# Performance work log

Hardware: AMD Instinct MI355X
Metric: run time of the kernel (lower is better)

The kernel has to match this reference:

```python
import jax, jax.numpy as jnp
import numpy as np

B, C, H, W = 2, 256, 64, 64
NH = 4          # num_heads -> ch = C // NH = 64
G = 32          # GroupNorm groups (normalization(channels))
EPS = 1e-5


def setup_inputs() -> dict:
    key = jax.random.key(0)
    ks = jax.random.split(key, 7)
    s = 1.0 / np.sqrt(C).astype(np.float32)
    return {
        "x": jax.random.normal(ks[0], (B, C, H, W), jnp.float32),
        "gn_scale": 1.0 + 0.02 * jax.random.normal(ks[1], (C,), jnp.float32),
        "gn_bias": 0.02 * jax.random.normal(ks[2], (C,), jnp.float32),
        "w_qkv": s * jax.random.normal(ks[3], (3 * C, C), jnp.float32),
        "b_qkv": jnp.zeros((3 * C,), jnp.float32),
        # NOTE: original zero-inits proj_out; we use random weights so the
        # attention path contributes to the output (meaningful baseline).
        "w_proj": s * jax.random.normal(ks[4], (C, C), jnp.float32),
        "b_proj": jnp.zeros((C,), jnp.float32),
    }


def reference(x, gn_scale, gn_bias, w_qkv, b_qkv, w_proj, b_proj):
    b, c = x.shape[0], x.shape[1]
    spatial = x.shape[2:]
    t = int(np.prod(spatial))
    xf = x.reshape(b, c, t)                      # [B, C, T]

    # GroupNorm(32) over (channels-in-group, T)
    xg = xf.reshape(b, G, c // G, t)
    mu = xg.mean(axis=(2, 3), keepdims=True)
    var = xg.var(axis=(2, 3), keepdims=True)
    xn = ((xg - mu) * jax.lax.rsqrt(var + EPS)).reshape(b, c, t)
    xn = xn * gn_scale[None, :, None] + gn_bias[None, :, None]

    # 1x1 conv -> qkv: [B, 3C, T]
    qkv = jnp.einsum('oc,bct->bot', w_qkv, xn) + b_qkv[None, :, None]

    # QKVAttentionLegacy: reshape (B*H, 3*ch, T) then split
    ch = c // NH
    qkv_h = qkv.reshape(b * NH, 3 * ch, t)
    q, k, v = jnp.split(qkv_h, 3, axis=1)        # each [B*H, ch, T]
    scale = 1.0 / np.sqrt(np.sqrt(ch)).astype(np.float32)
    w = jnp.einsum('bct,bcs->bts', q * scale, k * scale)   # [B*H, T, T]
    w = jax.nn.softmax(w.astype(jnp.float32), axis=-1).astype(qkv.dtype)
    a = jnp.einsum('bts,bcs->bct', w, v).reshape(b, c, t)  # [B, C, T]

    # proj 1x1 conv + residual
    h = jnp.einsum('oc,bct->bot', w_proj, a) + b_proj[None, :, None]
    return (xf + h).reshape(b, c, *spatial)
```

## Files before the change

### kernel.cpp

```cpp
#include <hip/hip_runtime.h>
#include <math.h>

#define T 4096
#define C 256
#define BATCH 2
#define NH 4
#define G 32
#define CPG 8
#define EPS 1e-5f
#define LOG2E 1.4426950408889634f
#define QSCALE (0.125f * LOG2E)
#define KSPLIT 4
#define KRANGE (T / KSPLIT)
#define BH (BATCH * NH)

typedef __attribute__((ext_vector_type(8))) short bfv8;
typedef __attribute__((ext_vector_type(4))) short bfv4;
typedef __attribute__((ext_vector_type(4))) float f32x4;
typedef __attribute__((ext_vector_type(16))) float f32x16;

static __device__ __forceinline__ short f2bf(float f) {
    union { float f; unsigned u; } v; v.f = f;
    return (short)((v.u + 0x7FFFu + ((v.u >> 16) & 1u)) >> 16);
}
static __device__ __forceinline__ short f2bf_fast(float f) {
    union { float f; unsigned u; } v; v.f = f;
    return (short)((v.u + 0x8000u) >> 16);
}
static __device__ __forceinline__ float bf2f(short s) {
    union { float f; unsigned u; } v; v.u = ((unsigned)(unsigned short)s) << 16;
    return v.f;
}

#if __has_builtin(__builtin_amdgcn_exp2f)
#define EXP2(x) __builtin_amdgcn_exp2f(x)
#else
#define EXP2(x) exp2f(x)
#endif

#define AS1 __attribute__((address_space(1)))
#define AS3 __attribute__((address_space(3)))
static __device__ __forceinline__ void gll16(const void* g, void* l) {
    __builtin_amdgcn_global_load_lds((const AS1 void*)g, (AS3 void*)l, 16, 0, 0);
}

__global__ __launch_bounds__(256) void prep_w(const float* __restrict__ wq,
                                              const float* __restrict__ wp,
                                              short* __restrict__ wqb,
                                              short* __restrict__ wpb) {
    int i = blockIdx.x * 256 + threadIdx.x;
    const int NQ = 768 * 256 / 4;
    float4 v; short* dst;
    if (i < NQ) { v = ((const float4*)wq)[i]; dst = wqb + i * 4; }
    else        { int j = i - NQ; v = ((const float4*)wp)[j]; dst = wpb + j * 4; }
    bfv4 o = { f2bf(v.x), f2bf(v.y), f2bf(v.z), f2bf(v.w) };
    *(bfv4*)dst = o;
}

__global__ __launch_bounds__(256) void gn_stats(const float* __restrict__ x,
                                                float* __restrict__ gnp) {
    const int blk = blockIdx.x;
    const int ts  = blockIdx.y;
    const int b = blk / G, g = blk % G;
    const float* xp = x + ((size_t)b * C + g * CPG) * T + ts * 1024;

    const int tid = threadIdx.x;
    float s = 0.f, ss = 0.f;
    #pragma unroll
    for (int u = 0; u < CPG; u++) {
        float4 v = ((const float4*)(xp + (size_t)u * T))[tid];
        s  += v.x + v.y + v.z + v.w;
        ss += v.x*v.x + v.y*v.y + v.z*v.z + v.w*v.w;
    }
    __shared__ float rs[256], rss[256];
    rs[tid] = s; rss[tid] = ss;
    __syncthreads();
    for (int off = 128; off > 0; off >>= 1) {
        if (tid < off) { rs[tid] += rs[tid+off]; rss[tid] += rss[tid+off]; }
        __syncthreads();
    }
    if (tid == 0) {
        gnp[(blk * 4 + ts) * 2 + 0] = rs[0];
        gnp[(blk * 4 + ts) * 2 + 1] = rss[0];
    }
}

__global__ __launch_bounds__(256) void gn_norm(const float* __restrict__ x,
                                               const float* __restrict__ scale,
                                               const float* __restrict__ bias,
                                               const float* __restrict__ gnp,
                                               short* __restrict__ xnT) {
    const int blk = blockIdx.x;
    const int ts  = blockIdx.y;
    const int b = blk / G, g = blk % G;
    const int c0 = g * CPG;
    const float* xp = x + ((size_t)b * C + c0) * T;

    float s = 0.f, ss = 0.f;
    #pragma unroll
    for (int i = 0; i < 4; i++) {
        s  += gnp[(blk * 4 + i) * 2 + 0];
        ss += gnp[(blk * 4 + i) * 2 + 1];
    }
    const float inv_n = 1.0f / (CPG * T);
    const float mu  = s * inv_n;
    const float var = ss * inv_n - mu * mu;
    const float rstd = rsqrtf(var + EPS);

    float sc[CPG], bi[CPG];
    #pragma unroll
    for (int u = 0; u < CPG; u++) {
        sc[u] = scale[c0+u] * rstd;
        bi[u] = bias[c0+u] - mu * sc[u];
    }

    const int t = ts * 1024 + threadIdx.x * 4;
    float vv[CPG][4];
    #pragma unroll
    for (int u = 0; u < CPG; u++) {
        float4 v = *(const float4*)&xp[(size_t)u * T + t];
        vv[u][0] = v.x * sc[u] + bi[u];
        vv[u][1] = v.y * sc[u] + bi[u];
        vv[u][2] = v.z * sc[u] + bi[u];
        vv[u][3] = v.w * sc[u] + bi[u];
    }
    #pragma unroll
    for (int j = 0; j < 4; j++) {
        bfv8 w = { f2bf(vv[0][j]), f2bf(vv[1][j]), f2bf(vv[2][j]), f2bf(vv[3][j]),
                   f2bf(vv[4][j]), f2bf(vv[5][j]), f2bf(vv[6][j]), f2bf(vv[7][j]) };
        *(bfv8*)&xnT[((size_t)b * T + t + j) * C + c0] = w;
    }
}

__global__ __launch_bounds__(256) void gemm_qkv(
    const short* __restrict__ wq,
    const float* __restrict__ bq,
    const short* __restrict__ xnT,
    short* __restrict__ qb, short* __restrict__ kb, short* __restrict__ vb)
{
    const int b  = blockIdx.z;
    const int t0 = blockIdx.x * 64;
    const int ot = blockIdx.y;
    const int h = ot / 3, part = ot % 3;
    const int o0 = ot * 64;

    __shared__ short sm[8192];
    short* Ab = sm;
    short* Bb = sm + 4096;

    const int tid = threadIdx.x, lane = tid & 63, wave = tid >> 6;
    const int col = lane & 15, quad = lane >> 4;
    const short* xb = xnT + (size_t)b * T * C;

    f32x4 acc[4];
    #pragma unroll
    for (int g = 0; g < 4; g++) { acc[g][0]=0.f; acc[g][1]=0.f; acc[g][2]=0.f; acc[g][3]=0.f; }

    for (int k0 = 0; k0 < C; k0 += 64) {
        __syncthreads();
        #pragma unroll
        for (int hh = 0; hh < 2; hh++) {
            gll16(wq + (size_t)(o0 + 16*wave + col) * C + k0 + hh*32 + quad*8,
                  Ab + (hh*4 + wave) * 512);
            gll16(xb + (size_t)(t0 + 16*wave + col) * C + k0 + hh*32 + quad*8,
                  Bb + (hh*4 + wave) * 512);
        }
        __syncthreads();
        #pragma unroll
        for (int hh = 0; hh < 2; hh++) {
            bfv8 af = *(const bfv8*)(Ab + (hh*4 + wave) * 512 + lane*8);
            #pragma unroll
            for (int g = 0; g < 4; g++) {
                bfv8 bf = *(const bfv8*)(Bb + (hh*4 + g) * 512 + lane*8);
                acc[g] = __builtin_amdgcn_mfma_f32_16x16x32_bf16(af, bf, acc[g], 0, 0, 0);
            }
        }
    }

    const int olocal = 16*wave + quad*4;
    float bias_r[4];
    #pragma unroll
    for (int r = 0; r < 4; r++) bias_r[r] = bq[o0 + olocal + r];
    const size_t hd = (size_t)(b * NH + h);

    if (part < 2) {
        short* dst = (part == 0 ? qb : kb) + hd * T * 64;
        const float sc = (part == 0) ? QSCALE : 1.0f;
        #pragma unroll
        for (int g = 0; g < 4; g++) {
            int t = t0 + 16*g + col;
            bfv4 w = { f2bf((acc[g][0] + bias_r[0]) * sc),
                       f2bf((acc[g][1] + bias_r[1]) * sc),
                       f2bf((acc[g][2] + bias_r[2]) * sc),
                       f2bf((acc[g][3] + bias_r[3]) * sc) };
            *(bfv4*)&dst[(size_t)t * 64 + olocal] = w;
        }
    } else {
        short* dst = vb + hd * 64 * T;
        #pragma unroll
        for (int g = 0; g < 4; g++)
            #pragma unroll
            for (int r = 0; r < 4; r++)
                dst[(size_t)(olocal + r) * T + t0 + 16*g + col] =
                    f2bf(acc[g][r] + bias_r[r]);
    }
}

__global__ __launch_bounds__(512, 4) void attn_kernel(
    const short* __restrict__ qb,
    const short* __restrict__ kb,
    const short* __restrict__ vb,
    short* __restrict__ opart,
    float* __restrict__ lp)
{
    __shared__ short smem[16384];
    const int bh = blockIdx.y;
    const int ks = blockIdx.z;
    const int t0 = blockIdx.x * 256;
    const int k0base = ks * KRANGE;
    const short* kbh = kb + (size_t)bh * T * 64;
    const short* vbh = vb + (size_t)bh * 64 * T;

    const int tid  = threadIdx.x;
    const int lane = tid & 63;
    const int wave = tid >> 6;
    const int klow = lane & 31;
    const int hi   = lane >> 5;
    const int swz  = klow & 7;

    const int q = t0 + wave*32 + klow;
    const short* qrow = qb + (size_t)bh * T * 64 + (size_t)q * 64;
    bfv8 qf[4];
    #pragma unroll
    for (int s = 0; s < 4; s++) qf[s] = *(const bfv8*)(qrow + s*16 + hi*8);

    f32x16 oacc[2];
    #pragma unroll
    for (int c = 0; c < 2; c++)
        #pragma unroll
        for (int r = 0; r < 16; r++) oacc[c][r] = 0.f;
    float lsum = 0.f;

    const int srow = wave*8 + (lane >> 3);
    const int schunk = lane & 7;
    #define STAGE_KV(buf, s0)                                                   \
        {                                                                       \
            short* kB = smem + (buf) * 8192 + wave * 512;                       \
            gll16(kbh + (size_t)((s0) + srow) * 64 + ((schunk ^ (srow&7))<<3),  \
                  kB);                                                          \
            gll16(vbh + (size_t)srow * T + (s0) + ((schunk ^ (srow&7))<<3),     \
                  kB + 4096);                                                   \
        }

    STAGE_KV(0, k0base)

    for (int it = 0; it < KRANGE/64; it++) {
        __syncthreads();
        if (it + 1 < KRANGE/64) STAGE_KV((it+1) & 1, k0base + (it+1)*64)

        const short* kvb = smem + (it & 1) * 8192;
        const short* kl = kvb + klow*64;
        const short* vl = kvb + 4096 + klow*64 + 4*hi;

        bfv8 pf[2][2];
        #pragma unroll
        for (int kt = 0; kt < 2; kt++) {
            f32x16 sacc;
            #pragma unroll
            for (int r = 0; r < 16; r++) sacc[r] = 0.f;
            #pragma unroll
            for (int s = 0; s < 4; s++) {
                bfv8 kf = *(const bfv8*)(kl + kt*2048 + (((2*s+hi) ^ swz) << 3));
                sacc = __builtin_amdgcn_mfma_f32_32x32x16_bf16(kf, qf[s], sacc, 0, 0, 0);
            }
            #pragma unroll
            for (int u = 0; u < 2; u++) {
                bfv8 pk;
                #pragma unroll
                for (int j = 0; j < 8; j++) {
                    float p = EXP2(sacc[u*8 + j]);
                    lsum += p;
                    pk[j] = f2bf_fast(p);
                }
                pf[kt][u] = pk;
            }
        }

        #pragma unroll
        for (int kc = 0; kc < 4; kc++) {
            #pragma unroll
            for (int c = 0; c < 2; c++) {
                bfv4 v0 = *(const bfv4*)(vl + c*2048 + (((2*kc)   ^ swz) << 3));
                bfv4 v1 = *(const bfv4*)(vl + c*2048 + (((2*kc+1) ^ swz) << 3));
                bfv8 vf = { v0[0], v0[1], v0[2], v0[3],
                            v1[0], v1[1], v1[2], v1[3] };
                oacc[c] = __builtin_amdgcn_mfma_f32_32x32x16_bf16(
                              vf, pf[kc>>1][kc&1], oacc[c], 0, 0, 0);
            }
        }
    }

    lsum += __shfl_xor(lsum, 32);

    const size_t rowbase = (size_t)(ks*BH + bh) * T + t0 + wave*32;
    short* opb = opart + (rowbase + klow) * 64;
    #pragma unroll
    for (int c = 0; c < 2; c++)
        #pragma unroll
        for (int u = 0; u < 4; u++) {
            bfv4 w = { f2bf(oacc[c][4*u+0]), f2bf(oacc[c][4*u+1]),
                       f2bf(oacc[c][4*u+2]), f2bf(oacc[c][4*u+3]) };
            *(bfv4*)(opb + c*32 + u*8 + hi*4) = w;
        }
    if (hi == 0) {
        lp[rowbase + klow] = lsum;
    }
}

__global__ __launch_bounds__(256) void gemm_proj(
    const short* __restrict__ wp,
    const float* __restrict__ bp,
    const short* __restrict__ opart,
    const float* __restrict__ lp,
    const float* __restrict__ x,
    float* __restrict__ out)
{
    const int b  = blockIdx.z;
    const int t0 = blockIdx.x * 64;
    const int o0 = blockIdx.y * 64;

    __shared__ short sm[8192];
    short* Ab = sm;
    short* Bb = sm + 4096;

    const int tid = threadIdx.x, lane = tid & 63, wave = tid >> 6;
    const int col = lane & 15, quad = lane >> 4;

    const int trow = t0 + 16*wave + col;
    float rl4[NH];
    #pragma unroll
    for (int hh = 0; hh < NH; hh++) {
        float ls = 0.f;
        #pragma unroll
        for (int ks = 0; ks < KSPLIT; ks++)
            ls += lp[((size_t)(ks*BH) + b*NH + hh) * T + trow];
        rl4[hh] = 1.0f / ls;
    }

    f32x4 acc[4];
    #pragma unroll
    for (int g = 0; g < 4; g++) { acc[g][0]=0.f; acc[g][1]=0.f; acc[g][2]=0.f; acc[g][3]=0.f; }

    for (int k0 = 0; k0 < C; k0 += 64) {
        __syncthreads();
        #pragma unroll
        for (int hh = 0; hh < 2; hh++) {
            gll16(wp + (size_t)(o0 + 16*wave + col) * C + k0 + hh*32 + quad*8,
                  Ab + (hh*4 + wave) * 512);
            const int chg = k0 + hh*32 + quad*8;
            const int hd = chg >> 6, chin = chg & 63;
            const short* ob = opart + (((size_t)(b*NH + hd)) * T + trow) * 64 + chin;
            float a8[8] = {0.f,0.f,0.f,0.f,0.f,0.f,0.f,0.f};
            #pragma unroll
            for (int ks = 0; ks < KSPLIT; ks++) {
                bfv8 v = *(const bfv8*)(ob + (size_t)ks * BH * T * 64);
                #pragma unroll
                for (int u = 0; u < 8; u++) a8[u] += bf2f(v[u]);
            }
            const float rl = rl4[hd];
            bfv8 pk;
            #pragma unroll
            for (int u = 0; u < 8; u++) pk[u] = f2bf(a8[u] * rl);
            *(bfv8*)(Bb + (hh*4 + wave) * 512 + lane*8) = pk;
        }
        __syncthreads();
        #pragma unroll
        for (int hh = 0; hh < 2; hh++) {
            bfv8 af = *(const bfv8*)(Ab + (hh*4 + wave) * 512 + lane*8);
            #pragma unroll
            for (int g = 0; g < 4; g++) {
                bfv8 bf = *(const bfv8*)(Bb + (hh*4 + g) * 512 + lane*8);
                acc[g] = __builtin_amdgcn_mfma_f32_16x16x32_bf16(af, bf, acc[g], 0, 0, 0);
            }
        }
    }

    const int olocal = 16*wave + quad*4;
    #pragma unroll
    for (int r = 0; r < 4; r++) {
        const int o = o0 + olocal + r;
        const float bias = bp[o];
        const size_t rowoff = ((size_t)b * C + o) * T;
        #pragma unroll
        for (int g = 0; g < 4; g++) {
            const size_t idx = rowoff + t0 + 16*g + col;
            out[idx] = acc[g][r] + bias + x[idx];
        }
    }
}

extern "C" void kernel_launch(void* const* d_in, const int* in_sizes, int n_in,
                              void* d_out, int out_size, void* d_ws, size_t ws_size,
                              hipStream_t stream) {
    (void)in_sizes; (void)n_in; (void)out_size; (void)ws_size;
    const float* x        = (const float*)d_in[0];
    const float* gn_scale = (const float*)d_in[1];
    const float* gn_bias  = (const float*)d_in[2];
    const float* w_qkv    = (const float*)d_in[3];
    const float* b_qkv    = (const float*)d_in[4];
    const float* w_proj   = (const float*)d_in[5];
    const float* b_proj   = (const float*)d_in[6];
    float* out = (float*)d_out;

    short* ws    = (short*)d_ws;
    short* qb    = ws;
    short* kb    = qb  + (size_t)BH * T * 64;
    short* vb    = kb  + (size_t)BH * T * 64;
    short* xnT   = vb  + (size_t)BH * T * 64;
    short* wqb   = xnT + (size_t)BATCH * T * C;
    short* wpb   = wqb + 768 * 256;
    short* opart = wpb + 256 * 256;
    float* lp    = (float*)(opart + (size_t)KSPLIT * BH * T * 64);
    float* gnp   = lp + (size_t)KSPLIT * BH * T;

    prep_w<<<dim3(256), 256, 0, stream>>>(w_qkv, w_proj, wqb, wpb);
    gn_stats<<<dim3(BATCH * G, 4), 256, 0, stream>>>(x, gnp);
    gn_norm<<<dim3(BATCH * G, 4), 256, 0, stream>>>(x, gn_scale, gn_bias, gnp, xnT);
    gemm_qkv<<<dim3(T/64, 12, BATCH), 256, 0, stream>>>(wqb, b_qkv, xnT, qb, kb, vb);
    attn_kernel<<<dim3(T/256, BH, KSPLIT), 512, 0, stream>>>(qb, kb, vb, opart, lp);
    gemm_proj<<<dim3(T/64, 4, BATCH), 256, 0, stream>>>(wpb, b_proj, opart, lp, x, out);
}
```

Measured before the change: 152.4 us.

## Double K/V tile to 128, interleave PV MFMAs with softmax, merge prep kernels

The attention kernel now stages 128-key K/V tiles instead of 64, doubling shared memory to 64KB. This halves the number of barrier/stage iterations, and V gets a 16-way swizzle to match the wider rows. The P·V MFMAs are issued right after each softmax sub-block rather than after all scores, and a packed v_cvt_pk_bf16_f32 conversion plus a two-wide sum replace scalar bf16 rounding. Weight conversion and GroupNorm stats are merged into one launch to cut a kernel launch. The larger LDS footprint may reduce occupancy under launch_bounds(512,4).

```diff
diff --git a/kernel.cpp b/kernel.cpp
--- a/kernel.cpp
+++ b/kernel.cpp
@@ -12,20 +12,19 @@
 #define QSCALE (0.125f * LOG2E)
 #define KSPLIT 4
 #define KRANGE (T / KSPLIT)
+#define KTILE 128
+#define NIT (KRANGE / KTILE)
 #define BH (BATCH * NH)
 
 typedef __attribute__((ext_vector_type(8))) short bfv8;
 typedef __attribute__((ext_vector_type(4))) short bfv4;
 typedef __attribute__((ext_vector_type(4))) float f32x4;
+typedef __attribute__((ext_vector_type(2))) float f32x2;
 typedef __attribute__((ext_vector_type(16))) float f32x16;
 
 static __device__ __forceinline__ short f2bf(float f) {
     union { float f; unsigned u; } v; v.f = f;
     return (short)((v.u + 0x7FFFu + ((v.u >> 16) & 1u)) >> 16);
-}
-static __device__ __forceinline__ short f2bf_fast(float f) {
-    union { float f; unsigned u; } v; v.f = f;
-    return (short)((v.u + 0x8000u) >> 16);
 }
 static __device__ __forceinline__ float bf2f(short s) {
     union { float f; unsigned u; } v; v.u = ((unsigned)(unsigned short)s) << 16;
@@ -44,27 +43,29 @@
     __builtin_amdgcn_global_load_lds((const AS1 void*)g, (AS3 void*)l, 16, 0, 0);
 }
 
-__global__ __launch_bounds__(256) void prep_w(const float* __restrict__ wq,
-                                              const float* __restrict__ wp,
-                                              short* __restrict__ wqb,
-                                              short* __restrict__ wpb) {
-    int i = blockIdx.x * 256 + threadIdx.x;
-    const int NQ = 768 * 256 / 4;
-    float4 v; short* dst;
-    if (i < NQ) { v = ((const float4*)wq)[i]; dst = wqb + i * 4; }
-    else        { int j = i - NQ; v = ((const float4*)wp)[j]; dst = wpb + j * 4; }
-    bfv4 o = { f2bf(v.x), f2bf(v.y), f2bf(v.z), f2bf(v.w) };
-    *(bfv4*)dst = o;
-}
-
-__global__ __launch_bounds__(256) void gn_stats(const float* __restrict__ x,
-                                                float* __restrict__ gnp) {
-    const int blk = blockIdx.x;
-    const int ts  = blockIdx.y;
+__global__ __launch_bounds__(256) void prep_stats(
+    const float* __restrict__ wq, const float* __restrict__ wp,
+    short* __restrict__ wqb, short* __restrict__ wpb,
+    const float* __restrict__ x, float* __restrict__ gnp)
+{
+    __shared__ float rs[256], rss[256];
+    const int bid = blockIdx.x;
+    const int tid = threadIdx.x;
+    if (bid < 256) {
+        int i = bid * 256 + tid;
+        const int NQ = 768 * 256 / 4;
+        float4 v; short* dst;
+        if (i < NQ) { v = ((const float4*)wq)[i]; dst = wqb + i * 4; }
+        else        { int j = i - NQ; v = ((const float4*)wp)[j]; dst = wpb + j * 4; }
+        bfv4 o = { f2bf(v.x), f2bf(v.y), f2bf(v.z), f2bf(v.w) };
+        *(bfv4*)dst = o;
+        return;
+    }
+    const int blk = (bid - 256) >> 2;
+    const int ts  = (bid - 256) & 3;
     const int b = blk / G, g = blk % G;
     const float* xp = x + ((size_t)b * C + g * CPG) * T + ts * 1024;
 
-    const int tid = threadIdx.x;
     float s = 0.f, ss = 0.f;
     #pragma unroll
     for (int u = 0; u < CPG; u++) {
@@ -72,7 +73,6 @@
         s  += v.x + v.y + v.z + v.w;
         ss += v.x*v.x + v.y*v.y + v.z*v.z + v.w*v.w;
     }
-    __shared__ float rs[256], rss[256];
     rs[tid] = s; rss[tid] = ss;
     __syncthreads();
     for (int off = 128; off > 0; off >>= 1) {
@@ -213,7 +213,7 @@
     short* __restrict__ opart,
     float* __restrict__ lp)
 {
-    __shared__ short smem[16384];
+    __shared__ short smem[32768];
     const int bh = blockIdx.y;
     const int ks = blockIdx.z;
     const int t0 = blockIdx.x * 256;
@@ -227,6 +227,7 @@
     const int klow = lane & 31;
     const int hi   = lane >> 5;
     const int swz  = klow & 7;
+    const int vswz = klow & 15;
 
     const int q = t0 + wave*32 + klow;
     const short* qrow = qb + (size_t)bh * T * 64 + (size_t)q * 64;
@@ -239,32 +240,39 @@
     for (int c = 0; c < 2; c++)
         #pragma unroll
         for (int r = 0; r < 16; r++) oacc[c][r] = 0.f;
-    float lsum = 0.f;
-
-    const int srow = wave*8 + (lane >> 3);
-    const int schunk = lane & 7;
+    f32x2 l2 = { 0.f, 0.f };
+
+    const int lr8  = lane >> 3, lc8  = lane & 7;
+    const int lr16 = lane >> 4, lc16 = lane & 15;
     #define STAGE_KV(buf, s0)                                                   \
         {                                                                       \
-            short* kB = smem + (buf) * 8192 + wave * 512;                       \
-            gll16(kbh + (size_t)((s0) + srow) * 64 + ((schunk ^ (srow&7))<<3),  \
-                  kB);                                                          \
-            gll16(vbh + (size_t)srow * T + (s0) + ((schunk ^ (srow&7))<<3),     \
-                  kB + 4096);                                                   \
+            short* base = smem + (buf) * 16384;                                 \
+            const int r0 = (wave*2+0)*8 + lr8;                                  \
+            const int r1 = (wave*2+1)*8 + lr8;                                  \
+            gll16(kbh + (size_t)((s0) + r0) * 64 + ((lc8 ^ (r0&7))<<3),         \
+                  base + (wave*2+0)*512);                                       \
+            gll16(kbh + (size_t)((s0) + r1) * 64 + ((lc8 ^ (r1&7))<<3),         \
+                  base + (wave*2+1)*512);                                       \
+            const int v0r = (wave*2+0)*4 + lr16;                                \
+            const int v1r = (wave*2+1)*4 + lr16;                                \
+            gll16(vbh + (size_t)v0r * T + (s0) + ((lc16 ^ (v0r&15))<<3),        \
+                  base + 8192 + (wave*2+0)*512);                                \
+            gll16(vbh + (size_t)v1r * T + (s0) + ((lc16 ^ (v1r&15))<<3),        \
+                  base + 8192 + (wave*2+1)*512);                                \
         }
 
     STAGE_KV(0, k0base)
 
-    for (int it = 0; it < KRANGE/64; it++) {
-        __syncthreads();
-        if (it + 1 < KRANGE/64) STAGE_KV((it+1) & 1, k0base + (it+1)*64)
-
-        const short* kvb = smem + (it & 1) * 8192;
+    for (int it = 0; it < NIT; it++) {
+        __syncthreads();
+        if (it + 1 < NIT) STAGE_KV((it+1) & 1, k0base + (it+1)*KTILE)
+
+        const short* kvb = smem + (it & 1) * 16384;
         const short* kl = kvb + klow*64;
-        const short* vl = kvb + 4096 + klow*64 + 4*hi;
-
-        bfv8 pf[2][2];
-        #pragma unroll
-        for (int kt = 0; kt < 2; kt++) {
+        const short* vl = kvb + 8192 + klow*128 + 4*hi;
+
+        #pragma unroll
+        for (int kt = 0; kt < 4; kt++) {
             f32x16 sacc;
             #pragma unroll
             for (int r = 0; r < 16; r++) sacc[r] = 0.f;
@@ -275,31 +283,32 @@
             }
             #pragma unroll
             for (int u = 0; u < 2; u++) {
-                bfv8 pk;
+                float p[8];
                 #pragma unroll
-                for (int j = 0; j < 8; j++) {
-                    float p = EXP2(sacc[u*8 + j]);
-                    lsum += p;
-                    pk[j] = f2bf_fast(p);
+                for (int j = 0; j < 8; j++) p[j] = EXP2(sacc[8*u + j]);
+                f32x2 pa = { p[0], p[1] }, pb = { p[2], p[3] };
+                f32x2 pc = { p[4], p[5] }, pd = { p[6], p[7] };
+                l2 += (pa + pb) + (pc + pd);
+                union { unsigned w[4]; bfv8 v; } pk_;
+                #pragma unroll
+                for (int w = 0; w < 4; w++)
+                    asm("v_cvt_pk_bf16_f32 %0, %1, %2"
+                        : "=v"(pk_.w[w]) : "v"(p[2*w]), "v"(p[2*w+1]));
+                const int kc = 2*kt + u;
+                #pragma unroll
+                for (int c = 0; c < 2; c++) {
+                    bfv4 v0 = *(const bfv4*)(vl + c*4096 + (((2*kc)   ^ vswz) << 3));
+                    bfv4 v1 = *(const bfv4*)(vl + c*4096 + (((2*kc+1) ^ vswz) << 3));
+                    bfv8 vf = { v0[0], v0[1], v0[2], v0[3],
+                                v1[0], v1[1], v1[2], v1[3] };
+                    oacc[c] = __builtin_amdgcn_mfma_f32_32x32x16_bf16(
+                                  vf, pk_.v, oacc[c], 0, 0, 0);
                 }
-                pf[kt][u] = pk;
             }
         }
-
-        #pragma unroll
-        for (int kc = 0; kc < 4; kc++) {
-            #pragma unroll
-            for (int c = 0; c < 2; c++) {
-                bfv4 v0 = *(const bfv4*)(vl + c*2048 + (((2*kc)   ^ swz) << 3));
-                bfv4 v1 = *(const bfv4*)(vl + c*2048 + (((2*kc+1) ^ swz) << 3));
-                bfv8 vf = { v0[0], v0[1], v0[2], v0[3],
-                            v1[0], v1[1], v1[2], v1[3] };
-                oacc[c] = __builtin_amdgcn_mfma_f32_32x32x16_bf16(
-                              vf, pf[kc>>1][kc&1], oacc[c], 0, 0, 0);
-            }
-        }
-    }
-
+    }
+
+    float lsum = l2[0] + l2[1];
     lsum += __shfl_xor(lsum, 32);
 
     const size_t rowbase = (size_t)(ks*BH + bh) * T + t0 + wave*32;
@@ -423,8 +432,7 @@
     float* lp    = (float*)(opart + (size_t)KSPLIT * BH * T * 64);
     float* gnp   = lp + (size_t)KSPLIT * BH * T;
 
-    prep_w<<<dim3(256), 256, 0, stream>>>(w_qkv, w_proj, wqb, wpb);
-    gn_stats<<<dim3(BATCH * G, 4), 256, 0, stream>>>(x, gnp);
+    prep_stats<<<dim3(512), 256, 0, stream>>>(w_qkv, w_proj, wqb, wpb, x, gnp);
     gn_norm<<<dim3(BATCH * G, 4), 256, 0, stream>>>(x, gn_scale, gn_bias, gnp, xnT);
     gemm_qkv<<<dim3(T/64, 12, BATCH), 256, 0, stream>>>(wqb, b_qkv, xnT, qb, kb, vb);
     attn_kernel<<<dim3(T/256, BH, KSPLIT), 512, 0, stream>>>(qb, kb, vb, opart, lp);
```

New measurement: 150.4 us. About the same (-1.3%).
